# Performance work log

Measured on AMD Instinct MI355X. Metric: run time of the kernel, lower is better.

Reference implementation:

```python
import jax, jax.numpy as jnp
import numpy as np

BATCH, ENC_IN, D_MODEL, D_STATE = 16, 256, 256, 16


def _mamba_params(key, d, d_conv, prefix):
    di = 2 * d  # expand = 2
    dtr = max(d // 16, 1)  # dt_rank = ceil(d_model/16)
    ks = jax.random.split(key, 6)
    return {
        prefix + '_in_w': jax.random.normal(ks[0], (2 * di, d), jnp.float32) * 0.02,
        prefix + '_conv_w': jax.random.normal(ks[1], (di, d_conv), jnp.float32) * 0.1,
        prefix + '_conv_b': jnp.zeros((di,), jnp.float32),
        prefix + '_xproj_w': jax.random.normal(ks[2], (dtr + 2 * D_STATE, di), jnp.float32) * 0.02,
        prefix + '_dt_w': jax.random.normal(ks[3], (di, dtr), jnp.float32) * 0.02,
        prefix + '_dt_b': jax.random.normal(ks[4], (di,), jnp.float32) * 0.02,
        prefix + '_Alog': jnp.log(jnp.broadcast_to(jnp.arange(1, D_STATE + 1, dtype=jnp.float32), (di, D_STATE))),
        prefix + '_Dp': jnp.ones((di,), jnp.float32),
        prefix + '_out_w': jax.random.normal(ks[5], (d, di), jnp.float32) * 0.02,
    }


def setup_inputs() -> dict:
    key = jax.random.key(0)
    k0, k1, k2, k3 = jax.random.split(key, 4)
    inp = {
        'x': jax.random.normal(k0, (BATCH, ENC_IN, D_MODEL), jnp.float32),
        'ln_g': jnp.ones((D_MODEL,), jnp.float32),
        'ln_b': jnp.zeros((D_MODEL,), jnp.float32),
    }
    inp.update(_mamba_params(k1, D_MODEL, 1, 'mf'))  # channel mixer fwd, d_conv=1
    inp.update(_mamba_params(k2, D_MODEL, 1, 'mb'))  # channel mixer bwd, d_conv=1
    inp.update(_mamba_params(k3, ENC_IN, 4, 'tm'))   # time mixer, d_conv=4
    return inp


def _mamba(x, in_w, conv_w, conv_b, xproj_w, dt_w, dt_b, Alog, Dp, out_w):
    # x: [B, L, d]  -> standard mamba_ssm Mamba block forward
    B, L, d = x.shape
    di = in_w.shape[0] // 2
    dtr = dt_w.shape[1]
    ds = D_STATE
    xz = x @ in_w.T                      # [B, L, 2*di]
    xs, z = xz[..., :di], xz[..., di:]
    # causal depthwise conv1d (pad left d_conv-1, truncate to L)
    K = conv_w.shape[1]
    xp = jnp.pad(xs, ((0, 0), (K - 1, 0), (0, 0)))
    xs = sum(conv_w[:, k] * xp[:, k:k + L, :] for k in range(K)) + conv_b
    xs = jax.nn.silu(xs)
    x_dbl = xs @ xproj_w.T               # [B, L, dtr + 2*ds]
    dt = x_dbl[..., :dtr]
    Bm = x_dbl[..., dtr:dtr + ds]        # [B, L, ds]
    Cm = x_dbl[..., dtr + ds:]           # [B, L, ds]
    delta = jax.nn.softplus(dt @ dt_w.T + dt_b)          # [B, L, di]
    A = -jnp.exp(Alog)                                   # [di, ds]
    dA = jnp.exp(delta[..., None] * A)                   # [B, L, di, ds]
    dBx = delta[..., None] * Bm[:, :, None, :] * xs[..., None]

    def step(h, inp):
        dAt, dBxt, Ct = inp              # [B,di,ds],[B,di,ds],[B,ds]
        h = dAt * h + dBxt
        return h, jnp.einsum('bds,bs->bd', h, Ct)

    h0 = jnp.zeros((B, di, ds), x.dtype)
    _, ys = jax.lax.scan(step, h0, (dA.transpose(1, 0, 2, 3), dBx.transpose(1, 0, 2, 3), Cm.transpose(1, 0, 2)))
    y = ys.transpose(1, 0, 2) + Dp * xs  # [B, L, di]
    y = y * jax.nn.silu(z)
    return y @ out_w.T                   # [B, L, d]


def _ln(x, g, b, eps=1e-5):
    m = x.mean(-1, keepdims=True)
    v = jnp.mean((x - m) ** 2, axis=-1, keepdims=True)
    return (x - m) / jnp.sqrt(v + eps) * g + b


def reference(x, ln_g, ln_b,
              mf_in_w, mf_conv_w, mf_conv_b, mf_xproj_w, mf_dt_w, mf_dt_b, mf_Alog, mf_Dp, mf_out_w,
              mb_in_w, mb_conv_w, mb_conv_b, mb_xproj_w, mb_dt_w, mb_dt_b, mb_Alog, mb_Dp, mb_out_w,
              tm_in_w, tm_conv_w, tm_conv_b, tm_xproj_w, tm_dt_w, tm_dt_b, tm_Alog, tm_Dp, tm_out_w):
    # BiMamba channel mixer
    y_f = _mamba(x, mf_in_w, mf_conv_w, mf_conv_b, mf_xproj_w, mf_dt_w, mf_dt_b, mf_Alog, mf_Dp, mf_out_w)
    y_b = _mamba(jnp.flip(x, axis=1), mb_in_w, mb_conv_w, mb_conv_b, mb_xproj_w, mb_dt_w, mb_dt_b, mb_Alog, mb_Dp, mb_out_w)
    y0 = y_f + jnp.flip(y_b, axis=1) + x
    y0 = _ln(y0, ln_g, ln_b)             # note: source uses norm1 both times
    # time mixer over the feature dimension
    y1 = y0.transpose(0, 2, 1)           # [B, d_model, enc_in]
    y1 = _mamba(y1, tm_in_w, tm_conv_w, tm_conv_b, tm_xproj_w, tm_dt_w, tm_dt_b, tm_Alog, tm_Dp, tm_out_w)
    y1 = y1.transpose(0, 2, 1)
    y2 = y1 * y0 + x
    return _ln(y2, ln_g, ln_b)
```

## Files before the change

kernel.cpp:

```cpp
#include <hip/hip_runtime.h>
#include <hip/hip_bf16.h>

typedef unsigned short u16;
typedef unsigned int   u32;

typedef short frag8 __attribute__((ext_vector_type(8)));
typedef float f32x4 __attribute__((ext_vector_type(4)));
typedef u16   u16x8 __attribute__((ext_vector_type(8)));
typedef u16   u16x4 __attribute__((ext_vector_type(4)));

__device__ __forceinline__ float bfb2f(u16 u) {
    return __uint_as_float(((u32)u) << 16);
}
__device__ __forceinline__ u16 f2bf(float v) {
    const u32 u = __float_as_uint(v);
    return (u16)((u + 0x7FFFu + ((u >> 16) & 1u)) >> 16);
}
__device__ __forceinline__ float silu_(float x) { return x / (1.f + __expf(-x)); }
__device__ __forceinline__ float softplus_fast(float x) {
    return (x > 20.f) ? x : __logf(1.f + __expf(x));
}

struct Cvt {
    const void* src[30];
    int dstoff[30];
    int n[30];
    int bstart[31];
};

__global__ __launch_bounds__(256) void convert_k(Cvt c, const u32* probe,
                                                 float* dst, u16* dstb) {
    const bool isb = (*probe != 0x3F800000u);
    const int bi = blockIdx.x;
    int i = 0;
    while (i < 29 && bi >= c.bstart[i + 1]) ++i;
    const int e = (bi - c.bstart[i]) * 256 + (int)threadIdx.x;
    if (e >= c.n[i]) return;
    const float v = isb ? bfb2f(((const u16*)c.src[i])[e])
                        : ((const float*)c.src[i])[e];
    dst[c.dstoff[i] + e]  = v;
    dstb[c.dstoff[i] + e] = f2bf(v);
}

__global__ __launch_bounds__(256, 2) void gemm1_fb_k(
    const u16* __restrict__ Xbf,
    const u16* __restrict__ Wf, const u16* __restrict__ Wb,
    const float* __restrict__ cwf, const float* __restrict__ cbf,
    const float* __restrict__ cwb, const float* __restrict__ cbb,
    u16* __restrict__ XSb_f, u16* __restrict__ XST_f, u16* __restrict__ ZST_f,
    u16* __restrict__ XSb_b, u16* __restrict__ XST_b, u16* __restrict__ ZST_b)
{
    __shared__ u16 tile[64][72];
    const int br = blockIdx.x >> 4;
    const int n0 = (blockIdx.x & 15) * 64;
    const u16* W = br ? Wb : Wf;
    const float* cw = br ? cwb : cwf;
    const float* cb = br ? cbb : cbf;
    u16* XSb = br ? XSb_b : XSb_f;
    u16* XST = br ? XST_b : XST_f;
    u16* ZST = br ? ZST_b : ZST_f;

    const int t = threadIdx.x;
    const int wave = t >> 6, lane = t & 63;
    const int l15 = lane & 15, quad = lane >> 4;
    const int mblk = blockIdx.y * 64;
    const int m0 = mblk + wave * 16;
    const u16* arow = Xbf + (size_t)(m0 + l15) * 256 + quad * 8;
    const u16* brow = W   + (size_t)(n0 + l15) * 256 + quad * 8;

    frag8 a[8];
    #pragma unroll
    for (int kk = 0; kk < 8; ++kk)
        a[kk] = *(const frag8*)(arow + kk * 32);
    frag8 b[8][4];
    #pragma unroll
    for (int kk = 0; kk < 8; ++kk)
        #pragma unroll
        for (int ni = 0; ni < 4; ++ni)
            b[kk][ni] = *(const frag8*)(brow + (size_t)ni * 16 * 256 + kk * 32);

    f32x4 acc[4] = {};
    #pragma unroll
    for (int kk = 0; kk < 8; ++kk)
        #pragma unroll
        for (int ni = 0; ni < 4; ++ni)
            acc[ni] = __builtin_amdgcn_mfma_f32_16x16x32_bf16(a[kk], b[kk][ni], acc[ni], 0, 0, 0);

    const bool isx = (n0 < 512);
    #pragma unroll
    for (int ni = 0; ni < 4; ++ni) {
        const int n = n0 + ni * 16 + l15;
        #pragma unroll
        for (int r = 0; r < 4; ++r) {
            const int m = mblk + wave * 16 + quad * 4 + r;
            const float v = acc[ni][r];
            const float s = isx ? silu_(fmaf(cw[n], v, cb[n])) : silu_(v);
            const u16 sb = f2bf(s);
            if (isx) XSb[(size_t)m * 512 + n] = sb;
            tile[n - n0][m - mblk] = sb;
        }
    }
    __syncthreads();
    const int b2 = mblk >> 8;
    const int l0 = mblk & 255;
    const int rown = t >> 2;
    const int chk  = (t & 3) * 16;
    const int dg = isx ? (n0 + rown) : (n0 - 512 + rown);
    u16* dst = (isx ? XST : ZST) + ((size_t)(b2 * 512 + dg)) * 256 + l0 + chk;
    *(u16x8*)dst       = *(const u16x8*)&tile[rown][chk];
    *(u16x8*)(dst + 8) = *(const u16x8*)&tile[rown][chk + 8];
}

__global__ __launch_bounds__(256, 2) void gemm1_tm_k(
    const u16* __restrict__ Ab, const u16* __restrict__ Bb,
    float* __restrict__ TMRAW, u16* __restrict__ ZST)
{
    __shared__ u16 tile[64][72];
    const int t = threadIdx.x;
    const int wave = t >> 6, lane = t & 63;
    const int l15 = lane & 15, quad = lane >> 4;
    const int mblk = blockIdx.y * 64;
    const int m0 = mblk + wave * 16;
    const int n0 = blockIdx.x * 64;
    const u16* arow = Ab + (size_t)(m0 + l15) * 256 + quad * 8;
    const u16* brow = Bb + (size_t)(n0 + l15) * 256 + quad * 8;

    frag8 a[8];
    #pragma unroll
    for (int kk = 0; kk < 8; ++kk)
        a[kk] = *(const frag8*)(arow + kk * 32);
    frag8 b[8][4];
    #pragma unroll
    for (int kk = 0; kk < 8; ++kk)
        #pragma unroll
        for (int ni = 0; ni < 4; ++ni)
            b[kk][ni] = *(const frag8*)(brow + (size_t)ni * 16 * 256 + kk * 32);

    f32x4 acc[4] = {};
    #pragma unroll
    for (int kk = 0; kk < 8; ++kk)
        #pragma unroll
        for (int ni = 0; ni < 4; ++ni)
            acc[ni] = __builtin_amdgcn_mfma_f32_16x16x32_bf16(a[kk], b[kk][ni], acc[ni], 0, 0, 0);

    const bool isx = (n0 < 512);
    if (isx) {
        #pragma unroll
        for (int ni = 0; ni < 4; ++ni) {
            const int n = n0 + ni * 16 + l15;
            #pragma unroll
            for (int r = 0; r < 4; ++r) {
                const int m = m0 + quad * 4 + r;
                TMRAW[(size_t)m * 512 + n] = acc[ni][r];
            }
        }
    } else {
        #pragma unroll
        for (int ni = 0; ni < 4; ++ni) {
            const int n = n0 + ni * 16 + l15;
            #pragma unroll
            for (int r = 0; r < 4; ++r) {
                const int m = m0 + quad * 4 + r;
                tile[n - n0][m - mblk] = f2bf(silu_(acc[ni][r]));
            }
        }
        __syncthreads();
        const int b2 = mblk >> 8;
        const int l0 = mblk & 255;
        const int rown = t >> 2;
        const int chk  = (t & 3) * 16;
        u16* dst = ZST + ((size_t)(b2 * 512 + (n0 - 512) + rown)) * 256 + l0 + chk;
        *(u16x8*)dst       = *(const u16x8*)&tile[rown][chk];
        *(u16x8*)(dst + 8) = *(const u16x8*)&tile[rown][chk + 8];
    }
}

__global__ __launch_bounds__(256, 2) void gemm_x_k(
    const u16* __restrict__ A0, const u16* __restrict__ B0, u16* __restrict__ O0,
    const u16* __restrict__ A1, const u16* __restrict__ B1, u16* __restrict__ O1)
{
    const int br = blockIdx.z;
    const u16* Ab = br ? A1 : A0;
    const u16* Bb = br ? B1 : B0;
    u16* out = br ? O1 : O0;
    const int t = threadIdx.x;
    const int wave = t >> 6, lane = t & 63;
    const int l15 = lane & 15, quad = lane >> 4;
    const int m0 = blockIdx.y * 64 + wave * 16;
    const int n0 = blockIdx.x * 16;
    const u16* arow = Ab + (size_t)(m0 + l15) * 512 + quad * 8;
    const u16* brow = Bb + (size_t)(n0 + l15) * 512 + quad * 8;

    frag8 a[16], b[16];
    #pragma unroll
    for (int kk = 0; kk < 16; ++kk) {
        a[kk] = *(const frag8*)(arow + kk * 32);
        b[kk] = *(const frag8*)(brow + kk * 32);
    }
    f32x4 acc0 = {}, acc1 = {};
    #pragma unroll
    for (int kk = 0; kk < 16; kk += 2) {
        acc0 = __builtin_amdgcn_mfma_f32_16x16x32_bf16(a[kk],     b[kk],     acc0, 0, 0, 0);
        acc1 = __builtin_amdgcn_mfma_f32_16x16x32_bf16(a[kk + 1], b[kk + 1], acc1, 0, 0, 0);
    }
    const f32x4 acc = acc0 + acc1;
    const int n = n0 + l15;
    #pragma unroll
    for (int r = 0; r < 4; ++r) {
        const int m = m0 + quad * 4 + r;
        out[(size_t)m * 48 + n] = f2bf(acc[r]);
    }
}

__global__ __launch_bounds__(256) void gemm_dt_k(
    const u16* __restrict__ A0, const u16* __restrict__ W0,
    const float* __restrict__ bias0, u16* __restrict__ O0,
    const u16* __restrict__ A1, const u16* __restrict__ W1,
    const float* __restrict__ bias1, u16* __restrict__ O1)
{
    __shared__ u16 tile[64][72];
    const int br = blockIdx.z;
    const u16* Ab = br ? A1 : A0;
    const u16* Wt = br ? W1 : W0;
    const float* bias = br ? bias1 : bias0;
    u16* out = br ? O1 : O0;

    const int t = threadIdx.x;
    const int wave = t >> 6, lane = t & 63;
    const int l15 = lane & 15, quad = lane >> 4;
    const int mblk = blockIdx.y * 64;
    const int m0 = mblk + wave * 16;
    const int n0 = blockIdx.x * 64;
    f32x4 acc[4] = {};
    frag8 a;
    #pragma unroll
    for (int j = 0; j < 8; ++j) a[j] = 0;
    if (quad < 2) a = *(const frag8*)(Ab + (size_t)(m0 + l15) * 48 + quad * 8);
    #pragma unroll
    for (int ni = 0; ni < 4; ++ni) {
        frag8 b;
        #pragma unroll
        for (int j = 0; j < 8; ++j) b[j] = 0;
        if (quad < 2) b = *(const frag8*)(Wt + (size_t)(n0 + ni * 16 + l15) * 16 + quad * 8);
        acc[ni] = __builtin_amdgcn_mfma_f32_16x16x32_bf16(a, b, acc[ni], 0, 0, 0);
    }
    #pragma unroll
    for (int ni = 0; ni < 4; ++ni) {
        const int n = n0 + ni * 16 + l15;
        #pragma unroll
        for (int r = 0; r < 4; ++r) {
            const int m = m0 + quad * 4 + r;
            tile[n - n0][m - mblk] = f2bf(softplus_fast(acc[ni][r] + bias[n]));
        }
    }
    __syncthreads();
    const int b  = mblk >> 8;
    const int l0 = mblk & 255;
    const int rown = t >> 2;
    const int chk  = (t & 3) * 16;
    u16* dst = out + ((size_t)(b * 512 + n0 + rown)) * 256 + l0 + chk;
    *(u16x8*)dst       = *(const u16x8*)&tile[rown][chk];
    *(u16x8*)(dst + 8) = *(const u16x8*)&tile[rown][chk + 8];
}

__global__ __launch_bounds__(256, 2) void gemm_o_k(
    const u16* __restrict__ A0, const u16* __restrict__ B0, float* __restrict__ O0,
    const u16* __restrict__ A1, const u16* __restrict__ B1, float* __restrict__ O1)
{
    const int br = blockIdx.z;
    const u16* Ab = br ? A1 : A0;
    const u16* Bb = br ? B1 : B0;
    float* out = br ? O1 : O0;
    const int t = threadIdx.x;
    const int wave = t >> 6, lane = t & 63;
    const int l15 = lane & 15, quad = lane >> 4;
    const int m0 = blockIdx.y * 64 + wave * 16;
    const int n0 = blockIdx.x * 32;
    const u16* arow = Ab + (size_t)(m0 + l15) * 512 + quad * 8;
    const u16* brow = Bb + (size_t)(n0 + l15) * 512 + quad * 8;

    frag8 a[16];
    #pragma unroll
    for (int kk = 0; kk < 16; ++kk)
        a[kk] = *(const frag8*)(arow + kk * 32);
    frag8 b[16][2];
    #pragma unroll
    for (int kk = 0; kk < 16; ++kk)
        #pragma unroll
        for (int ni = 0; ni < 2; ++ni)
            b[kk][ni] = *(const frag8*)(brow + (size_t)ni * 16 * 512 + kk * 32);

    f32x4 acc0[2] = {}, acc1[2] = {};
    #pragma unroll
    for (int kk = 0; kk < 16; kk += 2) {
        #pragma unroll
        for (int ni = 0; ni < 2; ++ni) {
            acc0[ni] = __builtin_amdgcn_mfma_f32_16x16x32_bf16(a[kk],     b[kk][ni],     acc0[ni], 0, 0, 0);
            acc1[ni] = __builtin_amdgcn_mfma_f32_16x16x32_bf16(a[kk + 1], b[kk + 1][ni], acc1[ni], 0, 0, 0);
        }
    }
    #pragma unroll
    for (int ni = 0; ni < 2; ++ni) {
        const f32x4 acc = acc0[ni] + acc1[ni];
        const int n = n0 + ni * 16 + l15;
        #pragma unroll
        for (int r = 0; r < 4; ++r) {
            const int m = m0 + quad * 4 + r;
            out[(size_t)m * 256 + n] = acc[r];
        }
    }
}

__global__ __launch_bounds__(256) void conv4t_k(
    const float* __restrict__ raw, const float* __restrict__ cw, const float* __restrict__ cb,
    u16* __restrict__ XSb, u16* __restrict__ XST)
{
    __shared__ u16 tile[64][72];
    const int b  = blockIdx.y;
    const int c0 = blockIdx.x * 64;
    const int cl = threadIdx.x & 63;
    const int seg = threadIdx.x >> 6;
    const int c = c0 + cl;
    const int tq = blockIdx.z * 64;
    const int tp0 = tq + seg * 16;
    const float w0 = cw[c * 4 + 0], w1 = cw[c * 4 + 1];
    const float w2 = cw[c * 4 + 2], w3 = cw[c * 4 + 3];
    const float bias = cb[c];
    float r3 = 0.f, r2 = 0.f, r1 = 0.f;
    if (tp0 > 0) {
        r3 = raw[((size_t)(b * 256 + tp0 - 3)) * 512 + c];
        r2 = raw[((size_t)(b * 256 + tp0 - 2)) * 512 + c];
        r1 = raw[((size_t)(b * 256 + tp0 - 1)) * 512 + c];
    }
    #pragma unroll
    for (int i = 0; i < 16; ++i) {
        const int tp = tp0 + i;
        const float cur = raw[((size_t)(b * 256 + tp)) * 512 + c];
        float acc = fmaf(w0, r3, bias);
        acc = fmaf(w1, r2, acc);
        acc = fmaf(w2, r1, acc);
        acc = fmaf(w3, cur, acc);
        const u16 sb = f2bf(silu_(acc));
        XSb[((size_t)(b * 256 + tp)) * 512 + c] = sb;
        tile[cl][tp - tq] = sb;
        r3 = r2; r2 = r1; r1 = cur;
    }
    __syncthreads();
    const int row = threadIdx.x >> 2;
    const int ch  = (threadIdx.x & 3) * 16;
    u16* dst = XST + ((size_t)(b * 512 + c0 + row)) * 256 + tq + ch;
    #pragma unroll
    for (int j = 0; j < 4; ++j)
        *(u16x4*)(dst + j * 4) = *(const u16x4*)&tile[row][ch + j * 4];
}

struct ScanSet {
    const u16 *xst, *zst, *dlt, *xdblb;
    const float *Alog, *Dp;
    u16* Y;
};

__global__ __launch_bounds__(256) void scan_fused_k(ScanSet s0, ScanSet s1, int branchStart)
{
    __shared__ float Ps[4354];
    __shared__ float Es[4354];
    const int br  = (blockIdx.x >= (u32)branchStart) ? 1 : 0;
    const ScanSet S = br ? s1 : s0;
    const int rev = br;
    const int bi2 = blockIdx.x - br * branchStart;
    const int b  = bi2 >> 6;
    const int d0 = (bi2 & 63) << 3;
    const int g  = threadIdx.x >> 3;
    const int cl = threadIdx.x & 7;
    const int d  = d0 + cl;

    bool fast = true;
    #pragma unroll
    for (int s = 0; s < 16; ++s) {
        const float a = -__expf(S.Alog[d * 16 + s]);
        fast &= (fabsf(a + (float)(s + 1)) < 1e-3f);
    }

    const size_t crow = ((size_t)(b * 512 + d)) * 256;
    const int lbase = rev ? (248 - g * 8) : (g * 8);
    const u16x8 xs8 = *(const u16x8*)(S.xst + crow + lbase);
    const u16x8 dl8 = *(const u16x8*)(S.dlt + crow + lbase);

    float h[16], P[16];
    #pragma unroll
    for (int s = 0; s < 16; ++s) { h[s] = 0.f; P[s] = 1.f; }
    float e1prod = 1.f;

    #pragma unroll
    for (int i = 0; i < 8; ++i) {
        const int j = rev ? (7 - i) : i;
        const int l = lbase + j;
        const size_t row = (size_t)(b * 256 + l);
        const float dl = bfb2f(dl8[j]);
        const float xv = bfb2f(xs8[j]);
        const u16x8 bv0 = *(const u16x8*)(S.xdblb + row * 48 + 16);
        const u16x8 bv1 = *(const u16x8*)(S.xdblb + row * 48 + 24);
        const float dlx = dl * xv;
        if (fast) {
            const float e1 = __expf(-dl);
            e1prod *= e1;
            const float e2 = e1 * e1, e4 = e2 * e2, e8 = e4 * e4;
            float pw[16];
            pw[0] = e1;        pw[1] = e2;        pw[2] = e2 * e1;   pw[3] = e4;
            pw[4] = e4 * e1;   pw[5] = e4 * e2;   pw[6] = e4 * pw[2]; pw[7] = e8;
            pw[8] = e8 * e1;   pw[9] = e8 * e2;   pw[10] = e8 * pw[2]; pw[11] = e8 * e4;
            pw[12] = e8 * pw[4]; pw[13] = e8 * pw[5]; pw[14] = e8 * pw[6]; pw[15] = e8 * e8;
            #pragma unroll
            for (int s = 0; s < 8; ++s)
                h[s] = fmaf(pw[s], h[s], dlx * bfb2f(bv0[s]));
            #pragma unroll
            for (int s = 8; s < 16; ++s)
                h[s] = fmaf(pw[s], h[s], dlx * bfb2f(bv1[s - 8]));
        } else {
            #pragma unroll
            for (int s = 0; s < 16; ++s) {
                const float As = -__expf(S.Alog[d * 16 + s]);
                const float dA = __expf(dl * As);
                P[s] *= dA;
                const float Bv = bfb2f((s < 8) ? bv0[s] : bv1[s - 8]);
                h[s] = fmaf(dA, h[s], dlx * Bv);
            }
        }
    }
    if (fast) {
        const float e1 = e1prod;
        const float e2 = e1 * e1, e4 = e2 * e2, e8 = e4 * e4;
        P[0] = e1;        P[1] = e2;        P[2] = e2 * e1;   P[3] = e4;
        P[4] = e4 * e1;   P[5] = e4 * e2;   P[6] = e4 * P[2]; P[7] = e8;
        P[8] = e8 * e1;   P[9] = e8 * e2;   P[10] = e8 * P[2]; P[11] = e8 * e4;
        P[12] = e8 * P[4]; P[13] = e8 * P[5]; P[14] = e8 * P[6]; P[15] = e8 * e8;
    }
    const int pbx = (g * 8 + cl) * 17;
    #pragma unroll
    for (int s = 0; s < 16; ++s) { Ps[pbx + s] = P[s]; Es[pbx + s] = h[s]; }
    __syncthreads();

    if (threadIdx.x < 128) {
        const int cl2 = threadIdx.x >> 4, s2 = threadIdx.x & 15;
        float hh = 0.f;
        #pragma unroll
        for (int gg = 0; gg < 32; ++gg) {
            const int o = (gg * 8 + cl2) * 17 + s2;
            const float tmp = Es[o];
            Es[o] = hh;
            hh = fmaf(Ps[o], hh, tmp);
        }
    }
    __syncthreads();

    #pragma unroll
    for (int s = 0; s < 16; ++s) h[s] = Es[pbx + s];
    const float Dpd = S.Dp[d];
    const u16x8 zs8 = *(const u16x8*)(S.zst + crow + lbase);
    #pragma unroll
    for (int i = 0; i < 8; ++i) {
        const int j = rev ? (7 - i) : i;
        const int l = lbase + j;
        const size_t row = (size_t)(b * 256 + l);
        const float dl = bfb2f(dl8[j]);
        const float xv = bfb2f(xs8[j]);
        const float zv = bfb2f(zs8[j]);
        const u16x8 bv0 = *(const u16x8*)(S.xdblb + row * 48 + 16);
        const u16x8 bv1 = *(const u16x8*)(S.xdblb + row * 48 + 24);
        const u16x8 cv0 = *(const u16x8*)(S.xdblb + row * 48 + 32);
        const u16x8 cv1 = *(const u16x8*)(S.xdblb + row * 48 + 40);
        const float dlx = dl * xv;
        float a0 = 0.f, a1 = 0.f, a2 = 0.f, a3 = 0.f;
        if (fast) {
            const float e1 = __expf(-dl);
            const float e2 = e1 * e1, e4 = e2 * e2, e8 = e4 * e4;
            float pw[16];
            pw[0] = e1;        pw[1] = e2;        pw[2] = e2 * e1;   pw[3] = e4;
            pw[4] = e4 * e1;   pw[5] = e4 * e2;   pw[6] = e4 * pw[2]; pw[7] = e8;
            pw[8] = e8 * e1;   pw[9] = e8 * e2;   pw[10] = e8 * pw[2]; pw[11] = e8 * e4;
            pw[12] = e8 * pw[4]; pw[13] = e8 * pw[5]; pw[14] = e8 * pw[6]; pw[15] = e8 * e8;
            #pragma unroll
            for (int s = 0; s < 16; ++s) {
                const float Bv = bfb2f((s < 8) ? bv0[s] : bv1[s - 8]);
                const float Cv = bfb2f((s < 8) ? cv0[s] : cv1[s - 8]);
                h[s] = fmaf(pw[s], h[s], dlx * Bv);
                const float hv = h[s] * Cv;
                if ((s & 3) == 0) a0 += hv;
                else if ((s & 3) == 1) a1 += hv;
                else if ((s & 3) == 2) a2 += hv;
                else a3 += hv;
            }
        } else {
            #pragma unroll
            for (int s = 0; s < 16; ++s) {
                const float As = -__expf(S.Alog[d * 16 + s]);
                const float dA = __expf(dl * As);
                const float Bv = bfb2f((s < 8) ? bv0[s] : bv1[s - 8]);
                const float Cv = bfb2f((s < 8) ? cv0[s] : cv1[s - 8]);
                h[s] = fmaf(dA, h[s], dlx * Bv);
                const float hv = h[s] * Cv;
                if ((s & 3) == 0) a0 += hv;
                else if ((s & 3) == 1) a1 += hv;
                else if ((s & 3) == 2) a2 += hv;
                else a3 += hv;
            }
        }
        const float acc = (a0 + a1) + (a2 + a3);
        S.Y[row * 512 + d] = f2bf((acc + Dpd * xv) * zv);
    }
}

__global__ __launch_bounds__(256) void combine_ln_k(
    const float* __restrict__ YF, const float* __restrict__ YB,
    const float* __restrict__ X, const float* __restrict__ g, const float* __restrict__ bb,
    float* __restrict__ Y0)
{
    const int m = blockIdx.x;
    const int c = threadIdx.x;
    const float v = YF[(size_t)m * 256 + c]
                  + YB[(size_t)m * 256 + c]
                  + X[(size_t)m * 256 + c];
    float s1 = v, s2 = v * v;
    #pragma unroll
    for (int off = 32; off > 0; off >>= 1) {
        s1 += __shfl_down(s1, off);
        s2 += __shfl_down(s2, off);
    }
    __shared__ float p1[4], p2[4];
    const int wave = c >> 6;
    if ((c & 63) == 0) { p1[wave] = s1; p2[wave] = s2; }
    __syncthreads();
    const float t1 = (p1[0] + p1[1]) + (p1[2] + p1[3]);
    const float t2 = (p2[0] + p2[1]) + (p2[2] + p2[3]);
    const float mean = t1 * (1.f / 256.f);
    const float var  = t2 * (1.f / 256.f) - mean * mean;
    const float inv  = rsqrtf(var + 1e-5f);
    Y0[(size_t)m * 256 + c] = (v - mean) * inv * g[c] + bb[c];
}

__global__ __launch_bounds__(256) void transpose_cast_k(
    const float* __restrict__ Y0, u16* __restrict__ Y0T)
{
    __shared__ float tile[64][65];
    const int b  = blockIdx.z;
    const int l0 = blockIdx.x * 64, c0 = blockIdx.y * 64;
    const int tc = threadIdx.x & 63;
    const int tr = threadIdx.x >> 6;
    #pragma unroll
    for (int j = 0; j < 16; ++j) {
        const int r = tr * 16 + j;
        tile[r][tc] = Y0[((size_t)(b * 256 + l0 + r)) * 256 + c0 + tc];
    }
    __syncthreads();
    #pragma unroll
    for (int j = 0; j < 16; ++j) {
        const int r = tr * 16 + j;
        Y0T[((size_t)(b * 256 + c0 + r)) * 256 + l0 + tc] = f2bf(tile[tc][r]);
    }
}

__global__ __launch_bounds__(256) void final_ln_k(
    const float* __restrict__ TMOUT, const float* __restrict__ Y0,
    const float* __restrict__ X, const float* __restrict__ g, const float* __restrict__ bb,
    float* __restrict__ out)
{
    const int m = blockIdx.x;
    const int c = threadIdx.x;
    const int b = m >> 8, l = m & 255;
    const float y1 = TMOUT[((size_t)(b * 256 + c)) * 256 + l];
    const float v = fmaf(y1, Y0[(size_t)m * 256 + c], X[(size_t)m * 256 + c]);
    float s1 = v, s2 = v * v;
    #pragma unroll
    for (int off = 32; off > 0; off >>= 1) {
        s1 += __shfl_down(s1, off);
        s2 += __shfl_down(s2, off);
    }
    __shared__ float p1[4], p2[4];
    const int wave = c >> 6;
    if ((c & 63) == 0) { p1[wave] = s1; p2[wave] = s2; }
    __syncthreads();
    const float t1 = (p1[0] + p1[1]) + (p1[2] + p1[3]);
    const float t2 = (p2[0] + p2[1]) + (p2[2] + p2[3]);
    const float mean = t1 * (1.f / 256.f);
    const float var  = t2 * (1.f / 256.f) - mean * mean;
    const float inv  = rsqrtf(var + 1e-5f);
    out[(size_t)m * 256 + c] = (v - mean) * inv * g[c] + bb[c];
}

extern "C" void kernel_launch(void* const* d_in, const int* in_sizes, int n_in,
                              void* d_out, int out_size, void* d_ws, size_t ws_size,
                              hipStream_t stream)
{
    float* ws = (float*)d_ws;

    Cvt c;
    int off = 0, blocks = 0;
    int doff[30];
    for (int i = 0; i < 30; ++i) {
        c.src[i]    = d_in[i];
        c.dstoff[i] = off;
        doff[i]     = off;
        c.n[i]      = in_sizes[i];
        c.bstart[i] = blocks;
        off    += in_sizes[i];
        blocks += (in_sizes[i] + 255) / 256;
    }
    c.bstart[30] = blocks;
    const int offa = (off + 7) & ~7;
    float* PARF = ws;
    u16*   PARB = (u16*)(ws + offa);
    float* ACT0 = ws + offa + offa / 2;

    convert_k<<<dim3(blocks), dim3(256), 0, stream>>>(c, (const u32*)d_in[1], PARF, PARB);

    auto P  = [&](int base, int o) -> const float* { return PARF + doff[base + o]; };
    auto Pb = [&](int base, int o) -> const u16*   { return PARB + doff[base + o]; };
    const float* X   = P(0, 0);
    const u16*   Xbf = Pb(0, 0);
    const float* lng = P(1, 0);
    const float* lnb = P(2, 0);

    u16* XSb_f   = (u16*)ACT0;
    u16* XSb_b   = XSb_f + 2097152;
    u16* XST_f   = XSb_b + 2097152;
    u16* XST_b   = XST_f + 2097152;
    u16* ZST_f   = XST_b + 2097152;
    u16* ZST_b   = ZST_f + 2097152;
    u16* DLT_f   = ZST_b + 2097152;
    u16* DLT_b   = DLT_f + 2097152;
    u16* Ybf_f   = DLT_b + 2097152;
    u16* Ybf_b   = Ybf_f + 2097152;
    u16* XDBLb_f = Ybf_b + 2097152;
    u16* XDBLb_b = XDBLb_f + 196608;
    u16* Y0T     = XDBLb_b + 196608;
    float* Y0    = (float*)(Y0T + 1048576);
    float* YF    = Y0 + 1048576;
    float* YB    = YF + 1048576;
    float* TMRAW = YB + 1048576;
    float* TMOUT = TMRAW + 2097152;

    const dim3 blk(256);
    const int mf = 3, mb = 12, tm = 21;

    gemm1_fb_k<<<dim3(32, 64), blk, 0, stream>>>(
        Xbf, Pb(mf, 0), Pb(mb, 0),
        P(mf, 1), P(mf, 2), P(mb, 1), P(mb, 2),
        XSb_f, XST_f, ZST_f, XSb_b, XST_b, ZST_b);
    gemm_x_k<<<dim3(3, 64, 2), blk, 0, stream>>>(
        XSb_f, Pb(mf, 3), XDBLb_f, XSb_b, Pb(mb, 3), XDBLb_b);
    gemm_dt_k<<<dim3(8, 64, 2), blk, 0, stream>>>(
        XDBLb_f, Pb(mf, 4), P(mf, 5), DLT_f,
        XDBLb_b, Pb(mb, 4), P(mb, 5), DLT_b);
    {
        ScanSet s0 { XST_f, ZST_f, DLT_f, XDBLb_f, P(mf, 6), P(mf, 7), Ybf_f };
        ScanSet s1 { XST_b, ZST_b, DLT_b, XDBLb_b, P(mb, 6), P(mb, 7), Ybf_b };
        scan_fused_k<<<dim3(2048), blk, 0, stream>>>(s0, s1, 1024);
    }
    gemm_o_k<<<dim3(8, 64, 2), blk, 0, stream>>>(
        Ybf_f, Pb(mf, 8), YF, Ybf_b, Pb(mb, 8), YB);

    combine_ln_k<<<dim3(4096), blk, 0, stream>>>(YF, YB, X, lng, lnb, Y0);
    transpose_cast_k<<<dim3(4, 4, 16), blk, 0, stream>>>(Y0, Y0T);

    gemm1_tm_k<<<dim3(16, 64), blk, 0, stream>>>(Y0T, Pb(tm, 0), TMRAW, ZST_f);
    conv4t_k<<<dim3(8, 16, 4), blk, 0, stream>>>(TMRAW, P(tm, 1), P(tm, 2), XSb_f, XST_f);
    gemm_x_k<<<dim3(3, 64, 1), blk, 0, stream>>>(
        XSb_f, Pb(tm, 3), XDBLb_f, XSb_f, Pb(tm, 3), XDBLb_f);
    gemm_dt_k<<<dim3(8, 64, 1), blk, 0, stream>>>(
        XDBLb_f, Pb(tm, 4), P(tm, 5), DLT_f,
        XDBLb_f, Pb(tm, 4), P(tm, 5), DLT_f);
    {
        ScanSet t0 { XST_f, ZST_f, DLT_f, XDBLb_f, P(tm, 6), P(tm, 7), Ybf_f };
        scan_fused_k<<<dim3(1024), blk, 0, stream>>>(t0, t0, 2048);
    }
    gemm_o_k<<<dim3(8, 64, 1), blk, 0, stream>>>(
        Ybf_f, Pb(tm, 8), TMOUT, Ybf_f, Pb(tm, 8), TMOUT);

    final_ln_k<<<dim3(4096), blk, 0, stream>>>(TMOUT, Y0, X, lng, lnb, (float*)d_out);
}
```

Before: 319.7 us.

## Stage in-proj weight tile in LDS via direct global-to-LDS loads, double M tile

Both first-stage in-projection GEMMs now load the 64x256 weight tile once per block into shared memory with global_load_lds and an XOR swizzle, instead of each wave holding all B fragments in registers. Each wave now computes 32 rows (block M tile 128), so the grid halves and weight traffic per output is reduced. Occupancy hint raised to 4 blocks/CU since register pressure drops. Costs 32KB LDS per block plus extra barriers, and the transpose tile reuses the same LDS buffer.

After: 283.2 us. 1.13x faster.

```diff
diff --git a/kernel.cpp b/kernel.cpp
--- a/kernel.cpp
+++ b/kernel.cpp
@@ -19,6 +19,11 @@
 __device__ __forceinline__ float silu_(float x) { return x / (1.f + __expf(-x)); }
 __device__ __forceinline__ float softplus_fast(float x) {
     return (x > 20.f) ? x : __logf(1.f + __expf(x));
+}
+__device__ __forceinline__ void gload_lds16(const void* g, void* l) {
+    __builtin_amdgcn_global_load_lds(
+        (const __attribute__((address_space(1))) void*)g,
+        (__attribute__((address_space(3))) void*)l, 16, 0, 0);
 }
 
 struct Cvt {
@@ -42,7 +47,7 @@
     dstb[c.dstoff[i] + e] = f2bf(v);
 }
 
-__global__ __launch_bounds__(256, 2) void gemm1_fb_k(
+__global__ __launch_bounds__(256, 4) void gemm1_fb_k(
     const u16* __restrict__ Xbf,
     const u16* __restrict__ Wf, const u16* __restrict__ Wb,
     const float* __restrict__ cwf, const float* __restrict__ cbf,
@@ -50,7 +55,9 @@
     u16* __restrict__ XSb_f, u16* __restrict__ XST_f, u16* __restrict__ ZST_f,
     u16* __restrict__ XSb_b, u16* __restrict__ XST_b, u16* __restrict__ ZST_b)
 {
-    __shared__ u16 tile[64][72];
+    __shared__ u16 Bs[16384];
+    u16 (*tile)[136] = (u16(*)[136])Bs;
+
     const int br = blockIdx.x >> 4;
     const int n0 = (blockIdx.x & 15) * 64;
     const u16* W = br ? Wb : Wf;
@@ -63,115 +70,153 @@
     const int t = threadIdx.x;
     const int wave = t >> 6, lane = t & 63;
     const int l15 = lane & 15, quad = lane >> 4;
-    const int mblk = blockIdx.y * 64;
-    const int m0 = mblk + wave * 16;
-    const u16* arow = Xbf + (size_t)(m0 + l15) * 256 + quad * 8;
-    const u16* brow = W   + (size_t)(n0 + l15) * 256 + quad * 8;
-
-    frag8 a[8];
-    #pragma unroll
-    for (int kk = 0; kk < 8; ++kk)
-        a[kk] = *(const frag8*)(arow + kk * 32);
-    frag8 b[8][4];
-    #pragma unroll
-    for (int kk = 0; kk < 8; ++kk)
-        #pragma unroll
-        for (int ni = 0; ni < 4; ++ni)
-            b[kk][ni] = *(const frag8*)(brow + (size_t)ni * 16 * 256 + kk * 32);
-
-    f32x4 acc[4] = {};
-    #pragma unroll
-    for (int kk = 0; kk < 8; ++kk)
-        #pragma unroll
-        for (int ni = 0; ni < 4; ++ni)
-            acc[ni] = __builtin_amdgcn_mfma_f32_16x16x32_bf16(a[kk], b[kk][ni], acc[ni], 0, 0, 0);
+    const int mblk = blockIdx.y * 128;
+
+    {
+        const char* Wp = (const char*)(W + (size_t)n0 * 256);
+        const int lane16 = lane * 16;
+        #pragma unroll
+        for (int j = 0; j < 8; ++j) {
+            const int s  = wave * 8 + j;
+            const int Lb = s * 1024 + lane16;
+            const int Ob = Lb ^ (((Lb >> 9) & 7) << 4);
+            gload_lds16(Wp + Ob, (char*)Bs + Lb);
+        }
+    }
+    asm volatile("s_waitcnt vmcnt(0)" ::: "memory");
+    __syncthreads();
+
+    const int m0w = mblk + wave * 32;
+    const u16* arow0 = Xbf + (size_t)(m0w + l15) * 256 + quad * 8;
+    const u16* arow1 = arow0 + 16 * 256;
+    f32x4 acc[2][4] = {};
+    #pragma unroll
+    for (int kk = 0; kk < 8; ++kk) {
+        const frag8 a0 = *(const frag8*)(arow0 + kk * 32);
+        const frag8 a1 = *(const frag8*)(arow1 + kk * 32);
+        #pragma unroll
+        for (int ni = 0; ni < 4; ++ni) {
+            const int bb = ((ni * 16 + l15) * 512 + kk * 64 + quad * 16)
+                         ^ ((l15 & 7) << 4);
+            const frag8 b = *(const frag8*)((const char*)Bs + bb);
+            acc[0][ni] = __builtin_amdgcn_mfma_f32_16x16x32_bf16(a0, b, acc[0][ni], 0, 0, 0);
+            acc[1][ni] = __builtin_amdgcn_mfma_f32_16x16x32_bf16(a1, b, acc[1][ni], 0, 0, 0);
+        }
+    }
+    __syncthreads();
 
     const bool isx = (n0 < 512);
     #pragma unroll
-    for (int ni = 0; ni < 4; ++ni) {
-        const int n = n0 + ni * 16 + l15;
-        #pragma unroll
-        for (int r = 0; r < 4; ++r) {
-            const int m = mblk + wave * 16 + quad * 4 + r;
-            const float v = acc[ni][r];
-            const float s = isx ? silu_(fmaf(cw[n], v, cb[n])) : silu_(v);
-            const u16 sb = f2bf(s);
-            if (isx) XSb[(size_t)m * 512 + n] = sb;
-            tile[n - n0][m - mblk] = sb;
-        }
-    }
-    __syncthreads();
-    const int b2 = mblk >> 8;
-    const int l0 = mblk & 255;
-    const int rown = t >> 2;
-    const int chk  = (t & 3) * 16;
-    const int dg = isx ? (n0 + rown) : (n0 - 512 + rown);
-    u16* dst = (isx ? XST : ZST) + ((size_t)(b2 * 512 + dg)) * 256 + l0 + chk;
-    *(u16x8*)dst       = *(const u16x8*)&tile[rown][chk];
-    *(u16x8*)(dst + 8) = *(const u16x8*)&tile[rown][chk + 8];
-}
-
-__global__ __launch_bounds__(256, 2) void gemm1_tm_k(
-    const u16* __restrict__ Ab, const u16* __restrict__ Bb,
-    float* __restrict__ TMRAW, u16* __restrict__ ZST)
-{
-    __shared__ u16 tile[64][72];
-    const int t = threadIdx.x;
-    const int wave = t >> 6, lane = t & 63;
-    const int l15 = lane & 15, quad = lane >> 4;
-    const int mblk = blockIdx.y * 64;
-    const int m0 = mblk + wave * 16;
-    const int n0 = blockIdx.x * 64;
-    const u16* arow = Ab + (size_t)(m0 + l15) * 256 + quad * 8;
-    const u16* brow = Bb + (size_t)(n0 + l15) * 256 + quad * 8;
-
-    frag8 a[8];
-    #pragma unroll
-    for (int kk = 0; kk < 8; ++kk)
-        a[kk] = *(const frag8*)(arow + kk * 32);
-    frag8 b[8][4];
-    #pragma unroll
-    for (int kk = 0; kk < 8; ++kk)
-        #pragma unroll
-        for (int ni = 0; ni < 4; ++ni)
-            b[kk][ni] = *(const frag8*)(brow + (size_t)ni * 16 * 256 + kk * 32);
-
-    f32x4 acc[4] = {};
-    #pragma unroll
-    for (int kk = 0; kk < 8; ++kk)
-        #pragma unroll
-        for (int ni = 0; ni < 4; ++ni)
-            acc[ni] = __builtin_amdgcn_mfma_f32_16x16x32_bf16(a[kk], b[kk][ni], acc[ni], 0, 0, 0);
-
-    const bool isx = (n0 < 512);
-    if (isx) {
+    for (int mi = 0; mi < 2; ++mi) {
         #pragma unroll
         for (int ni = 0; ni < 4; ++ni) {
             const int n = n0 + ni * 16 + l15;
             #pragma unroll
             for (int r = 0; r < 4; ++r) {
-                const int m = m0 + quad * 4 + r;
-                TMRAW[(size_t)m * 512 + n] = acc[ni][r];
+                const int ml = wave * 32 + mi * 16 + quad * 4 + r;
+                const int m  = mblk + ml;
+                const float v = acc[mi][ni][r];
+                const float s = isx ? silu_(fmaf(cw[n], v, cb[n])) : silu_(v);
+                const u16 sb = f2bf(s);
+                if (isx) XSb[(size_t)m * 512 + n] = sb;
+                tile[ni * 16 + l15][ml] = sb;
             }
         }
+    }
+    __syncthreads();
+
+    const int b2 = mblk >> 8;
+    const int l0 = mblk & 255;
+    const int rown = t >> 2;
+    const int cc  = (t & 3) * 32;
+    const int dg = isx ? (n0 + rown) : (n0 - 512 + rown);
+    u16* dst = (isx ? XST : ZST) + ((size_t)(b2 * 512 + dg)) * 256 + l0 + cc;
+    #pragma unroll
+    for (int p = 0; p < 4; ++p)
+        *(u16x8*)(dst + p * 8) = *(const u16x8*)&tile[rown][cc + p * 8];
+}
+
+__global__ __launch_bounds__(256, 4) void gemm1_tm_k(
+    const u16* __restrict__ Ab, const u16* __restrict__ Bbg,
+    float* __restrict__ TMRAW, u16* __restrict__ ZST)
+{
+    __shared__ u16 Bs[16384];
+    u16 (*tile)[136] = (u16(*)[136])Bs;
+
+    const int t = threadIdx.x;
+    const int wave = t >> 6, lane = t & 63;
+    const int l15 = lane & 15, quad = lane >> 4;
+    const int mblk = blockIdx.y * 128;
+    const int n0 = blockIdx.x * 64;
+
+    {
+        const char* Wp = (const char*)(Bbg + (size_t)n0 * 256);
+        const int lane16 = lane * 16;
+        #pragma unroll
+        for (int j = 0; j < 8; ++j) {
+            const int s  = wave * 8 + j;
+            const int Lb = s * 1024 + lane16;
+            const int Ob = Lb ^ (((Lb >> 9) & 7) << 4);
+            gload_lds16(Wp + Ob, (char*)Bs + Lb);
+        }
+    }
+    asm volatile("s_waitcnt vmcnt(0)" ::: "memory");
+    __syncthreads();
+
+    const int m0w = mblk + wave * 32;
+    const u16* arow0 = Ab + (size_t)(m0w + l15) * 256 + quad * 8;
+    const u16* arow1 = arow0 + 16 * 256;
+    f32x4 acc[2][4] = {};
+    #pragma unroll
+    for (int kk = 0; kk < 8; ++kk) {
+        const frag8 a0 = *(const frag8*)(arow0 + kk * 32);
+        const frag8 a1 = *(const frag8*)(arow1 + kk * 32);
+        #pragma unroll
+        for (int ni = 0; ni < 4; ++ni) {
+            const int bb = ((ni * 16 + l15) * 512 + kk * 64 + quad * 16)
+                         ^ ((l15 & 7) << 4);
+            const frag8 b = *(const frag8*)((const char*)Bs + bb);
+            acc[0][ni] = __builtin_amdgcn_mfma_f32_16x16x32_bf16(a0, b, acc[0][ni], 0, 0, 0);
+            acc[1][ni] = __builtin_amdgcn_mfma_f32_16x16x32_bf16(a1, b, acc[1][ni], 0, 0, 0);
+        }
+    }
+
+    const bool isx = (n0 < 512);
+    if (isx) {
+        #pragma unroll
+        for (int mi = 0; mi < 2; ++mi) {
+            #pragma unroll
+            for (int ni = 0; ni < 4; ++ni) {
+                const int n = n0 + ni * 16 + l15;
+                #pragma unroll
+                for (int r = 0; r < 4; ++r) {
+                    const int m = mblk + wave * 32 + mi * 16 + quad * 4 + r;
+                    TMRAW[(size_t)m * 512 + n] = acc[mi][ni][r];
+                }
+            }
+        }
     } else {
-        #pragma unroll
-        for (int ni = 0; ni < 4; ++ni) {
-            const int n = n0 + ni * 16 + l15;
+        __syncthreads();
+        #pragma unroll
+        for (int mi = 0; mi < 2; ++mi) {
             #pragma unroll
-            for (int r = 0; r < 4; ++r) {
-                const int m = m0 + quad * 4 + r;
-                tile[n - n0][m - mblk] = f2bf(silu_(acc[ni][r]));
+            for (int ni = 0; ni < 4; ++ni) {
+                #pragma unroll
+                for (int r = 0; r < 4; ++r) {
+                    const int ml = wave * 32 + mi * 16 + quad * 4 + r;
+                    tile[ni * 16 + l15][ml] = f2bf(silu_(acc[mi][ni][r]));
+                }
             }
         }
         __syncthreads();
         const int b2 = mblk >> 8;
         const int l0 = mblk & 255;
         const int rown = t >> 2;
-        const int chk  = (t & 3) * 16;
-        u16* dst = ZST + ((size_t)(b2 * 512 + (n0 - 512) + rown)) * 256 + l0 + chk;
-        *(u16x8*)dst       = *(const u16x8*)&tile[rown][chk];
-        *(u16x8*)(dst + 8) = *(const u16x8*)&tile[rown][chk + 8];
+        const int cc  = (t & 3) * 32;
+        u16* dst = ZST + ((size_t)(b2 * 512 + (n0 - 512) + rown)) * 256 + l0 + cc;
+        #pragma unroll
+        for (int p = 0; p < 4; ++p)
+            *(u16x8*)(dst + p * 8) = *(const u16x8*)&tile[rown][cc + p * 8];
     }
 }
 
@@ -642,7 +687,7 @@
     const dim3 blk(256);
     const int mf = 3, mb = 12, tm = 21;
 
-    gemm1_fb_k<<<dim3(32, 64), blk, 0, stream>>>(
+    gemm1_fb_k<<<dim3(32, 32), blk, 0, stream>>>(
         Xbf, Pb(mf, 0), Pb(mb, 0),
         P(mf, 1), P(mf, 2), P(mb, 1), P(mb, 2),
         XSb_f, XST_f, ZST_f, XSb_b, XST_b, ZST_b);
@@ -662,7 +707,7 @@
     combine_ln_k<<<dim3(4096), blk, 0, stream>>>(YF, YB, X, lng, lnb, Y0);
     transpose_cast_k<<<dim3(4, 4, 16), blk, 0, stream>>>(Y0, Y0T);
 
-    gemm1_tm_k<<<dim3(16, 64), blk, 0, stream>>>(Y0T, Pb(tm, 0), TMRAW, ZST_f);
+    gemm1_tm_k<<<dim3(16, 32), blk, 0, stream>>>(Y0T, Pb(tm, 0), TMRAW, ZST_f);
     conv4t_k<<<dim3(8, 16, 4), blk, 0, stream>>>(TMRAW, P(tm, 1), P(tm, 2), XSb_f, XST_f);
     gemm_x_k<<<dim3(3, 64, 1), blk, 0, stream>>>(
         XSb_f, Pb(tm, 3), XDBLb_f, XSb_f, Pb(tm, 3), XDBLb_f);
```
